# Kernel optimization log

Hardware: AMD Instinct MI355X
Metric: run time of the kernel (lower is better)

The kernel has to match this reference:

```python
import jax, jax.numpy as jnp
import numpy as np

R, M1, N1, M2, N2 = 8, 32, 64, 24, 48  # m1*m2=768, n1*n2=3072
B, S = 4, 1024


def setup_inputs() -> dict:
    key = jax.random.key(0)
    ks = jax.random.split(key, 8)
    x = jax.random.normal(ks[0], (B, S, M1 * M2), dtype=jnp.float32)
    std = 0.001
    A1 = jax.random.normal(ks[1], (R, N1, M1), dtype=jnp.float32) * std
    B1 = jax.random.normal(ks[2], (R, M2, N2), dtype=jnp.float32) * std
    A2 = jax.random.normal(ks[3], (R, M1, N1), dtype=jnp.float32) * std
    B2 = jax.random.normal(ks[4], (R, N2, M2), dtype=jnp.float32) * std
    b1 = jnp.zeros((N1 * N2,), dtype=jnp.float32)
    b2 = jnp.zeros((M1 * M2,), dtype=jnp.float32)
    p_inv = jax.random.permutation(ks[5], M1 * M2).astype(jnp.int64)
    q = jax.random.permutation(ks[6], M1 * M2).astype(jnp.int64)
    return {"x": x, "A1": A1, "B1": B1, "A2": A2, "B2": B2,
            "b1": b1, "b2": b2, "p_inv": p_inv, "q": q}


def reference(x, A1, B1, A2, B2, b1, b2, p_inv, q):
    b, s, _ = x.shape
    bs = b * s
    # permutation gather, then first Kronecker block
    xp = x[:, :, p_inv].reshape(-1, M2)                      # [bs*m1, m2]
    Bx = jnp.einsum('km,rmn->rkn', xp, B1)                   # [r, bs*m1, n2]
    Bx = Bx.reshape(R, bs, M1, N2)
    h = jnp.einsum('rnm,rbmj->bnj', A1, Bx)                  # [bs, n1, n2]
    h = h.reshape(b, s, N1 * N2) + b1
    h = jax.nn.gelu(h, approximate=False)
    # second Kronecker block
    hp = h.reshape(-1, N2)                                   # [bs*n1, n2]
    Bx2 = jnp.einsum('km,rmn->rkn', hp, B2)                  # [r, bs*n1, m2]
    Bx2 = Bx2.reshape(R, bs, N1, M2)
    out = jnp.einsum('rnm,rbmj->bnj', A2, Bx2)               # [bs, m1, m2]
    out = (out.reshape(b, s, M1 * M2) + b2)[:, :, q]         # permutation scatter
    return out
```

## Files before the change

kernel.cpp:

```cpp
#include <hip/hip_runtime.h>
#include <cmath>

namespace {

typedef _Float16 half8_t __attribute__((ext_vector_type(8)));
typedef _Float16 half4_t __attribute__((ext_vector_type(4)));
typedef float    f32x4_t __attribute__((ext_vector_type(4)));

constexpr int R_ = 8, M1_ = 32, N1_ = 64, M2_ = 24, N2_ = 48;
constexpr int DIN = 768;
constexpr int T_TOK = 8;
constexpr int NTHREADS = 512;

constexpr int W1_OFF = 0;
constexpr int W2_OFF = 30720;
constexpr int W3_OFF = 47104;
constexpr int W4_OFF = 63488;
constexpr int W_TOTAL = 75776;

constexpr int T1A_H = 0;
constexpr int T1B_H = 15360;
constexpr int XP_H  = 15360;
constexpr int HG_H  = 0;
constexpr int ZP_H  = 27648;
constexpr int LDS_BYTES = (27648 + 12544) * 2;

__global__ void prep_weights(const float* __restrict__ A1, const float* __restrict__ B1,
                             const float* __restrict__ A2, const float* __restrict__ B2,
                             _Float16* __restrict__ W)
{
    const int idx = blockIdx.x * 256 + threadIdx.x;
    if (idx >= W_TOTAL) return;
    float v;
    if (idx < W2_OFF) {
        int k = idx % 40, j = (idx / 40) % 48, r = idx / 1920;
        v = (k < 24) ? B1[(r * 24 + k) * 48 + j] : 0.0f;
    } else if (idx < W3_OFF) {
        int t = idx - W2_OFF;
        int rk = t & 255, n1 = t >> 8;
        v = A1[((rk >> 5) * 64 + n1) * 32 + (rk & 31)];
    } else if (idx < W4_OFF) {
        v = A2[idx - W3_OFF];
    } else {
        int t = idx - W4_OFF;
        int k = t % 384, m2 = t / 384;
        v = (m2 < 24) ? B2[k * 24 + m2] : 0.0f;
    }
    W[idx] = (_Float16)(v * 64.0f);
}

__global__ __launch_bounds__(NTHREADS, 4)
void kn_mfma(const float* __restrict__ x,
             const float* __restrict__ b1,
             const float* __restrict__ b2,
             const int* __restrict__ p_inv,
             const int* __restrict__ q,
             const _Float16* __restrict__ W,
             float* __restrict__ out)
{
    extern __shared__ char smem[];
    _Float16* ldsH = (_Float16*)smem;
    float*    ldsF = (float*)smem;

    const int tid  = threadIdx.x;
    const int lane = tid & 63;
    const int w    = __builtin_amdgcn_readfirstlane(tid >> 6);
    const int quad = lane >> 4;
    const int l16  = lane & 15;

    const long tokBase = (long)blockIdx.x * T_TOK;
    const bool idx64 = (p_inv[1] == 0 && p_inv[3] == 0);

    {
        const int t = w;
        const float* xrow = x + (size_t)(tokBase + t) * DIN;
        #pragma unroll
        for (int c = 0; c < 12; ++c) {
            const int kIdx = c * 64 + lane;
            const int pidx = idx64 ? p_inv[2 * kIdx] : p_inv[kIdx];
            const int i = kIdx / 24, m2 = kIdx - i * 24;
            ldsH[XP_H + (t * 32 + i) * 40 + m2] = (_Float16)xrow[pidx];
        }
        const int r0 = tid >> 1, c0 = 24 + (tid & 1) * 8;
        *(half8_t*)&ldsH[XP_H + r0 * 40 + c0] = half8_t{0, 0, 0, 0, 0, 0, 0, 0};
    }
    __syncthreads();

    const f32x4_t zero4 = {0.f, 0.f, 0.f, 0.f};

    const half8_t xp0 = *(const half8_t*)&ldsH[XP_H + (32 * w + l16) * 40 + quad * 8];
    const half8_t xp1 = *(const half8_t*)&ldsH[XP_H + (32 * w + 16 + l16) * 40 + quad * 8];

    f32x4_t hacc[12];
    #pragma unroll
    for (int u = 0; u < 12; ++u) hacc[u] = zero4;

    auto stage1 = [&](int rr) {
        _Float16* t1 = ldsH + ((rr & 1) ? T1B_H : T1A_H);
        #pragma unroll
        for (int ct = 0; ct < 3; ++ct) {
            const half8_t bf = *(const half8_t*)&W[W1_OFF + (rr * 48 + ct * 16 + l16) * 40 + quad * 8];
            const f32x4_t c0 = __builtin_amdgcn_mfma_f32_16x16x32_f16(xp0, bf, zero4, 0, 0, 0);
            const f32x4_t c1 = __builtin_amdgcn_mfma_f32_16x16x32_f16(xp1, bf, zero4, 0, 0, 0);
            const int s = w * 48 + ct * 16 + l16;
            half4_t p;
            p[0] = (_Float16)c0[0]; p[1] = (_Float16)c0[1];
            p[2] = (_Float16)c0[2]; p[3] = (_Float16)c0[3];
            *(half4_t*)&t1[s * 40 + quad * 4] = p;
            p[0] = (_Float16)c1[0]; p[1] = (_Float16)c1[1];
            p[2] = (_Float16)c1[2]; p[3] = (_Float16)c1[3];
            *(half4_t*)&t1[s * 40 + 16 + quad * 4] = p;
        }
    };

    auto stage2 = [&](int rr) {
        const _Float16* t1 = ldsH + ((rr & 1) ? T1B_H : T1A_H);
        const half8_t af = *(const half8_t*)&W[W2_OFF + ((w & 3) * 16 + l16) * 256 + rr * 32 + quad * 8];
        #pragma unroll
        for (int u = 0; u < 12; ++u) {
            const int ct = (w >> 2) + 2 * u;
            const half8_t bf = *(const half8_t*)&t1[(ct * 16 + l16) * 40 + quad * 8];
            hacc[u] = __builtin_amdgcn_mfma_f32_16x16x32_f16(af, bf, hacc[u], 0, 0, 0);
        }
    };

    stage1(0);
    __syncthreads();
    for (int r = 0; r < R_; ++r) {
        stage2(r);
        if (r + 1 < R_) stage1(r + 1);
        __syncthreads();
    }

    {
        const float inv4096 = 1.0f / 4096.0f;
        #pragma unroll
        for (int u = 0; u < 12; ++u) {
            const int ct = (w >> 2) + 2 * u;
            const int s  = ct * 16 + l16;
            const int n2 = s % 48;
            const int n1b = (w & 3) * 16 + quad * 4;
            half4_t p;
            #pragma unroll
            for (int rg = 0; rg < 4; ++rg) {
                const float hv = hacc[u][rg] * inv4096 + b1[(n1b + rg) * 48 + n2];
                float g;
                if (__builtin_expect(fabsf(hv) < 0.04f, 1)) {
                    g = fmaf(0.3989422804f * hv, hv, 0.5f * hv);
                } else {
                    g = 0.5f * hv * (1.0f + erff(hv * 0.70710678118654752f));
                }
                p[rg] = (_Float16)(g * 4096.0f);
            }
            *(half4_t*)&ldsH[HG_H + s * 72 + n1b] = p;
        }
    }

    const int kh  = w >> 2;
    const int rt4 = (w >> 1) & 1;
    const int ct4 = w & 1;
    const float sc = 1.0f / 16777216.0f;

    half8_t w3f[2][2];
    #pragma unroll
    for (int e = 0; e < 2; ++e)
        #pragma unroll
        for (int kk = 0; kk < 2; ++kk)
            w3f[e][kk] = *(const half8_t*)&W[W3_OFF + (w * 32 + e * 16 + l16) * 64 + kk * 32 + quad * 8];

    half8_t w4f[6];
    #pragma unroll
    for (int kk = 0; kk < 6; ++kk)
        w4f[kk] = *(const half8_t*)&W[W4_OFF + (ct4 * 16 + l16) * 384 + kh * 192 + kk * 32 + quad * 8];

    const int  qa = idx64 ? q[2 * tid] : q[tid];
    const float ba = b2[qa];
    const bool has2 = tid < DIN - 512;
    int qb = 0; float bb = 0.f;
    if (has2) {
        qb = idx64 ? q[2 * (512 + tid)] : q[512 + tid];
        bb = b2[qb];
    }
    __syncthreads();

    for (int tt = 0; tt < T_TOK; ++tt) {
        f32x4_t zc[6];
        #pragma unroll
        for (int u = 0; u < 6; ++u) zc[u] = zero4;
        #pragma unroll
        for (int ct = 0; ct < 3; ++ct)
            #pragma unroll
            for (int kk = 0; kk < 2; ++kk) {
                const half8_t af = *(const half8_t*)&ldsH[HG_H + (tt * 48 + ct * 16 + l16) * 72 + kk * 32 + quad * 8];
                #pragma unroll
                for (int e = 0; e < 2; ++e) {
                    const int u = ct * 2 + e;
                    zc[u] = __builtin_amdgcn_mfma_f32_16x16x32_f16(af, w3f[e][kk], zc[u], 0, 0, 0);
                }
            }
        #pragma unroll
        for (int ct = 0; ct < 3; ++ct)
            #pragma unroll
            for (int e = 0; e < 2; ++e) {
                const int u = ct * 2 + e;
                half4_t p;
                p[0] = (_Float16)zc[u][0]; p[1] = (_Float16)zc[u][1];
                p[2] = (_Float16)zc[u][2]; p[3] = (_Float16)zc[u][3];
                *(half4_t*)&ldsH[ZP_H + (e * 16 + l16) * 392 + w * 48 + ct * 16 + quad * 4] = p;
            }
        __syncthreads();

        f32x4_t oc = zero4;
        #pragma unroll
        for (int kk = 0; kk < 6; ++kk) {
            const half8_t zf = *(const half8_t*)&ldsH[ZP_H + (rt4 * 16 + l16) * 392 + kh * 192 + kk * 32 + quad * 8];
            oc = __builtin_amdgcn_mfma_f32_16x16x32_f16(w4f[kk], zf, oc, 0, 0, 0);
        }
        {
            const int m2b = ct4 * 16 + quad * 4;
            if (m2b < M2_) {
                *(f32x4_t*)&ldsF[1728 * tt + kh * 768 + (rt4 * 16 + l16) * 24 + m2b] = oc;
            }
        }
        __syncthreads();

        {
            const float* Pb = ldsF + 1728 * tt;
            float* orow = out + (size_t)(tokBase + tt) * DIN;
            orow[tid] = (Pb[qa] + Pb[768 + qa]) * sc + ba;
            if (has2)
                orow[512 + tid] = (Pb[qb] + Pb[768 + qb]) * sc + bb;
        }
    }
}

}

extern "C" void kernel_launch(void* const* d_in, const int* in_sizes, int n_in,
                              void* d_out, int out_size, void* d_ws, size_t ws_size,
                              hipStream_t stream) {
    const float* x   = (const float*)d_in[0];
    const float* A1  = (const float*)d_in[1];
    const float* B1  = (const float*)d_in[2];
    const float* A2  = (const float*)d_in[3];
    const float* B2  = (const float*)d_in[4];
    const float* b1  = (const float*)d_in[5];
    const float* b2  = (const float*)d_in[6];
    const int*   piv = (const int*)d_in[7];
    const int*   q   = (const int*)d_in[8];
    float* out = (float*)d_out;
    _Float16* Wws = (_Float16*)d_ws;

    const int tokens = in_sizes[0] / DIN;
    const int grid   = tokens / T_TOK;

    prep_weights<<<(W_TOTAL + 255) / 256, 256, 0, stream>>>(A1, B1, A2, B2, Wws);

    (void)hipFuncSetAttribute((const void*)kn_mfma,
                              hipFuncAttributeMaxDynamicSharedMemorySize,
                              LDS_BYTES);
    kn_mfma<<<grid, NTHREADS, LDS_BYTES, stream>>>(x, b1, b2, piv, q, Wws, out);
}
```

Measured before the change: 111.2 us.

## Prefetch weight fragments two rounds ahead and drop initial block barrier

Weight fragments for stage1 and stage2 are now loaded from global memory into registers one to two rank iterations ahead, using a double-buffered register set, so their latency overlaps MFMA work. The loop is fully unrolled so the register buffers can be indexed statically. Each wave now zero-pads only its own token's rows of the gathered input tile, and the first __syncthreads is removed because each wave reads only the rows it wrote. This raises register pressure, which could reduce occupancy.

Result: no change. 110.1 us (-1.0%).

```diff
diff --git a/kernel.cpp b/kernel.cpp
--- a/kernel.cpp
+++ b/kernel.cpp
@@ -72,19 +72,17 @@
     const bool idx64 = (p_inv[1] == 0 && p_inv[3] == 0);
 
     {
-        const int t = w;
-        const float* xrow = x + (size_t)(tokBase + t) * DIN;
+        const float* xrow = x + (size_t)(tokBase + w) * DIN;
         #pragma unroll
         for (int c = 0; c < 12; ++c) {
             const int kIdx = c * 64 + lane;
             const int pidx = idx64 ? p_inv[2 * kIdx] : p_inv[kIdx];
             const int i = kIdx / 24, m2 = kIdx - i * 24;
-            ldsH[XP_H + (t * 32 + i) * 40 + m2] = (_Float16)xrow[pidx];
-        }
-        const int r0 = tid >> 1, c0 = 24 + (tid & 1) * 8;
+            ldsH[XP_H + (w * 32 + i) * 40 + m2] = (_Float16)xrow[pidx];
+        }
+        const int r0 = w * 32 + (lane >> 1), c0 = 24 + (lane & 1) * 8;
         *(half8_t*)&ldsH[XP_H + r0 * 40 + c0] = half8_t{0, 0, 0, 0, 0, 0, 0, 0};
     }
-    __syncthreads();
 
     const f32x4_t zero4 = {0.f, 0.f, 0.f, 0.f};
 
@@ -95,13 +93,19 @@
     #pragma unroll
     for (int u = 0; u < 12; ++u) hacc[u] = zero4;
 
-    auto stage1 = [&](int rr) {
+    auto w1load = [&](int rr, int ct) -> half8_t {
+        return *(const half8_t*)&W[W1_OFF + (rr * 48 + ct * 16 + l16) * 40 + quad * 8];
+    };
+    auto w2load = [&](int rr) -> half8_t {
+        return *(const half8_t*)&W[W2_OFF + ((w & 3) * 16 + l16) * 256 + rr * 32 + quad * 8];
+    };
+
+    auto stage1 = [&](int rr, const half8_t* w1f) {
         _Float16* t1 = ldsH + ((rr & 1) ? T1B_H : T1A_H);
         #pragma unroll
         for (int ct = 0; ct < 3; ++ct) {
-            const half8_t bf = *(const half8_t*)&W[W1_OFF + (rr * 48 + ct * 16 + l16) * 40 + quad * 8];
-            const f32x4_t c0 = __builtin_amdgcn_mfma_f32_16x16x32_f16(xp0, bf, zero4, 0, 0, 0);
-            const f32x4_t c1 = __builtin_amdgcn_mfma_f32_16x16x32_f16(xp1, bf, zero4, 0, 0, 0);
+            const f32x4_t c0 = __builtin_amdgcn_mfma_f32_16x16x32_f16(xp0, w1f[ct], zero4, 0, 0, 0);
+            const f32x4_t c1 = __builtin_amdgcn_mfma_f32_16x16x32_f16(xp1, w1f[ct], zero4, 0, 0, 0);
             const int s = w * 48 + ct * 16 + l16;
             half4_t p;
             p[0] = (_Float16)c0[0]; p[1] = (_Float16)c0[1];
@@ -113,9 +117,8 @@
         }
     };
 
-    auto stage2 = [&](int rr) {
+    auto stage2 = [&](int rr, half8_t af) {
         const _Float16* t1 = ldsH + ((rr & 1) ? T1B_H : T1A_H);
-        const half8_t af = *(const half8_t*)&W[W2_OFF + ((w & 3) * 16 + l16) * 256 + rr * 32 + quad * 8];
         #pragma unroll
         for (int u = 0; u < 12; ++u) {
             const int ct = (w >> 2) + 2 * u;
@@ -124,11 +127,25 @@
         }
     };
 
-    stage1(0);
+    half8_t w1x[2][3];
+    half8_t w2x[2];
+    #pragma unroll
+    for (int ct = 0; ct < 3; ++ct) w1x[0][ct] = w1load(0, ct);
+    w2x[0] = w2load(0);
+    stage1(0, w1x[0]);
+    #pragma unroll
+    for (int ct = 0; ct < 3; ++ct) w1x[1][ct] = w1load(1, ct);
+    w2x[1] = w2load(1);
     __syncthreads();
+    #pragma unroll
     for (int r = 0; r < R_; ++r) {
-        stage2(r);
-        if (r + 1 < R_) stage1(r + 1);
+        stage2(r, w2x[r & 1]);
+        if (r + 1 < R_) stage1(r + 1, w1x[(r + 1) & 1]);
+        if (r + 2 < R_) {
+            #pragma unroll
+            for (int ct = 0; ct < 3; ++ct) w1x[r & 1][ct] = w1load(r + 2, ct);
+            w2x[r & 1] = w2load(r + 2);
+        }
         __syncthreads();
     }
 
```

## Give each wave a private LDS slab and drop block barriers in first Kronecker stage

Applied to the files above, without the earlier changes.

Each wave now gathers its own token's permuted input into a private LDS slab and computes the whole first Kronecker block for that token, covering all 64 n1 and 48 n2 outputs. The cross-wave split of stage 2, the double-buffered T1 regions and the per-rank __syncthreads are removed, since within-wave LDS ordering is enough. The GELU output is written into rows that fall inside the wave's own slab, so the existing LDS layout is reused. The aim is to cut block-wide barrier stalls in the rank loop. In exchange, waves lose cross-wave overlap and now rely on full unrolling for ILP.

Measured after the change: 119.9 us. 1.08x slower.

```diff
diff --git a/kernel.cpp b/kernel.cpp
--- a/kernel.cpp
+++ b/kernel.cpp
@@ -18,9 +18,8 @@
 constexpr int W4_OFF = 63488;
 constexpr int W_TOTAL = 75776;
 
-constexpr int T1A_H = 0;
-constexpr int T1B_H = 15360;
-constexpr int XP_H  = 15360;
+constexpr int SLAB  = 3456;
+constexpr int T1_L  = 1280;
 constexpr int HG_H  = 0;
 constexpr int ZP_H  = 27648;
 constexpr int LDS_BYTES = (27648 + 12544) * 2;
@@ -71,89 +70,80 @@
     const long tokBase = (long)blockIdx.x * T_TOK;
     const bool idx64 = (p_inv[1] == 0 && p_inv[3] == 0);
 
+    _Float16* slab = ldsH + w * SLAB;
+
     {
-        const int t = w;
-        const float* xrow = x + (size_t)(tokBase + t) * DIN;
+        const float* xrow = x + (size_t)(tokBase + w) * DIN;
         #pragma unroll
         for (int c = 0; c < 12; ++c) {
             const int kIdx = c * 64 + lane;
             const int pidx = idx64 ? p_inv[2 * kIdx] : p_inv[kIdx];
             const int i = kIdx / 24, m2 = kIdx - i * 24;
-            ldsH[XP_H + (t * 32 + i) * 40 + m2] = (_Float16)xrow[pidx];
-        }
-        const int r0 = tid >> 1, c0 = 24 + (tid & 1) * 8;
-        *(half8_t*)&ldsH[XP_H + r0 * 40 + c0] = half8_t{0, 0, 0, 0, 0, 0, 0, 0};
-    }
-    __syncthreads();
+            slab[i * 40 + m2] = (_Float16)xrow[pidx];
+        }
+        const int r0 = lane >> 1, c0 = 24 + (lane & 1) * 8;
+        *(half8_t*)&slab[r0 * 40 + c0] = half8_t{0, 0, 0, 0, 0, 0, 0, 0};
+    }
 
     const f32x4_t zero4 = {0.f, 0.f, 0.f, 0.f};
 
-    const half8_t xp0 = *(const half8_t*)&ldsH[XP_H + (32 * w + l16) * 40 + quad * 8];
-    const half8_t xp1 = *(const half8_t*)&ldsH[XP_H + (32 * w + 16 + l16) * 40 + quad * 8];
+    const half8_t xp0 = *(const half8_t*)&slab[l16 * 40 + quad * 8];
+    const half8_t xp1 = *(const half8_t*)&slab[(16 + l16) * 40 + quad * 8];
 
     f32x4_t hacc[12];
     #pragma unroll
     for (int u = 0; u < 12; ++u) hacc[u] = zero4;
 
-    auto stage1 = [&](int rr) {
-        _Float16* t1 = ldsH + ((rr & 1) ? T1B_H : T1A_H);
+    _Float16* t1 = slab + T1_L;
+
+    #pragma unroll
+    for (int r = 0; r < R_; ++r) {
         #pragma unroll
         for (int ct = 0; ct < 3; ++ct) {
-            const half8_t bf = *(const half8_t*)&W[W1_OFF + (rr * 48 + ct * 16 + l16) * 40 + quad * 8];
+            const half8_t bf = *(const half8_t*)&W[W1_OFF + (r * 48 + ct * 16 + l16) * 40 + quad * 8];
             const f32x4_t c0 = __builtin_amdgcn_mfma_f32_16x16x32_f16(xp0, bf, zero4, 0, 0, 0);
             const f32x4_t c1 = __builtin_amdgcn_mfma_f32_16x16x32_f16(xp1, bf, zero4, 0, 0, 0);
-            const int s = w * 48 + ct * 16 + l16;
             half4_t p;
             p[0] = (_Float16)c0[0]; p[1] = (_Float16)c0[1];
             p[2] = (_Float16)c0[2]; p[3] = (_Float16)c0[3];
-            *(half4_t*)&t1[s * 40 + quad * 4] = p;
+            *(half4_t*)&t1[(ct * 16 + l16) * 40 + quad * 4] = p;
             p[0] = (_Float16)c1[0]; p[1] = (_Float16)c1[1];
             p[2] = (_Float16)c1[2]; p[3] = (_Float16)c1[3];
-            *(half4_t*)&t1[s * 40 + 16 + quad * 4] = p;
-        }
-    };
-
-    auto stage2 = [&](int rr) {
-        const _Float16* t1 = ldsH + ((rr & 1) ? T1B_H : T1A_H);
-        const half8_t af = *(const half8_t*)&W[W2_OFF + ((w & 3) * 16 + l16) * 256 + rr * 32 + quad * 8];
-        #pragma unroll
-        for (int u = 0; u < 12; ++u) {
-            const int ct = (w >> 2) + 2 * u;
-            const half8_t bf = *(const half8_t*)&t1[(ct * 16 + l16) * 40 + quad * 8];
-            hacc[u] = __builtin_amdgcn_mfma_f32_16x16x32_f16(af, bf, hacc[u], 0, 0, 0);
-        }
-    };
-
-    stage1(0);
-    __syncthreads();
-    for (int r = 0; r < R_; ++r) {
-        stage2(r);
-        if (r + 1 < R_) stage1(r + 1);
-        __syncthreads();
+            *(half4_t*)&t1[(ct * 16 + l16) * 40 + 16 + quad * 4] = p;
+        }
+        #pragma unroll
+        for (int a = 0; a < 4; ++a) {
+            const half8_t af = *(const half8_t*)&W[W2_OFF + (a * 16 + l16) * 256 + r * 32 + quad * 8];
+            #pragma unroll
+            for (int c = 0; c < 3; ++c) {
+                const half8_t bf = *(const half8_t*)&t1[(c * 16 + l16) * 40 + quad * 8];
+                hacc[a * 3 + c] = __builtin_amdgcn_mfma_f32_16x16x32_f16(af, bf, hacc[a * 3 + c], 0, 0, 0);
+            }
+        }
     }
 
     {
         const float inv4096 = 1.0f / 4096.0f;
         #pragma unroll
-        for (int u = 0; u < 12; ++u) {
-            const int ct = (w >> 2) + 2 * u;
-            const int s  = ct * 16 + l16;
-            const int n2 = s % 48;
-            const int n1b = (w & 3) * 16 + quad * 4;
-            half4_t p;
-            #pragma unroll
-            for (int rg = 0; rg < 4; ++rg) {
-                const float hv = hacc[u][rg] * inv4096 + b1[(n1b + rg) * 48 + n2];
-                float g;
-                if (__builtin_expect(fabsf(hv) < 0.04f, 1)) {
-                    g = fmaf(0.3989422804f * hv, hv, 0.5f * hv);
-                } else {
-                    g = 0.5f * hv * (1.0f + erff(hv * 0.70710678118654752f));
+        for (int a = 0; a < 4; ++a)
+            #pragma unroll
+            for (int c = 0; c < 3; ++c) {
+                const int n2  = c * 16 + l16;
+                const int n1b = a * 16 + quad * 4;
+                half4_t p;
+                #pragma unroll
+                for (int rg = 0; rg < 4; ++rg) {
+                    const float hv = hacc[a * 3 + c][rg] * inv4096 + b1[(n1b + rg) * 48 + n2];
+                    float g;
+                    if (__builtin_expect(fabsf(hv) < 0.04f, 1)) {
+                        g = fmaf(0.3989422804f * hv, hv, 0.5f * hv);
+                    } else {
+                        g = 0.5f * hv * (1.0f + erff(hv * 0.70710678118654752f));
+                    }
+                    p[rg] = (_Float16)(g * 4096.0f);
                 }
-                p[rg] = (_Float16)(g * 4096.0f);
-            }
-            *(half4_t*)&ldsH[HG_H + s * 72 + n1b] = p;
-        }
+                *(half4_t*)&ldsH[HG_H + (w * 48 + n2) * 72 + n1b] = p;
+            }
     }
 
     const int kh  = w >> 2;
```
